# Kernel tuning notes

Hardware: AMD Instinct MI355X
Metric: run time of the kernel (lower is better)

Reference implementation:

```python
import jax, jax.numpy as jnp
import numpy as np

T = 0.5  # sharpening temperature
M, N, DK, DV = 8192, 8192, 512, 512


def setup_inputs() -> dict:
    key = jax.random.key(0)
    kq, kk, kv = jax.random.split(key, 3)
    Q = jax.random.normal(kq, (M, DK), dtype=jnp.float32)
    K = jax.random.normal(kk, (N, DK), dtype=jnp.float32)
    V = jax.random.normal(kv, (N, DV), dtype=jnp.float32)
    return {"Q": Q, "K": K, "V": V}


def reference(Q, K, V):
    d_k = K.shape[1]
    scores = jnp.matmul(Q, K.T) / np.sqrt(d_k)          # (m, n)
    attn = jax.nn.softmax(scores, axis=-1)              # (m, n)
    # sharpen: p^(1/T), renormalize over keys (dim=1 for 2D == last axis)
    u = jnp.power(attn, 1.0 / T)
    attn = u / jnp.sum(u, axis=1, keepdims=True)
    return jnp.matmul(attn, V)                          # (m, d_v)
```

## Files before the change

kernel.cpp:

```cpp
#include <hip/hip_runtime.h>

typedef unsigned short u16;
typedef __attribute__((ext_vector_type(8))) short bf16x8;
typedef __attribute__((ext_vector_type(4))) float f32x4;
typedef __attribute__((ext_vector_type(4))) u16 u16x4;

#define MFMA16(a, b, c) __builtin_amdgcn_mfma_f32_16x16x32_bf16(a, b, c, 0, 0, 0)

__device__ __forceinline__ u16 f2bf(float f) {
    union { float f; unsigned u; } v; v.f = f;
    unsigned r = (v.u + 0x7FFFu + ((v.u >> 16) & 1u)) >> 16;
    return (u16)r;
}

__device__ __forceinline__ void gload_lds16(const void* g, void* l) {
    __builtin_amdgcn_global_load_lds((const __attribute__((address_space(1))) void*)g,
                                     (__attribute__((address_space(3))) void*)l, 16, 0, 0);
}

__global__ __launch_bounds__(256) void cvt_kernel(const float* __restrict__ src,
                                                  u16* __restrict__ dst, int n4, float scale) {
    int i = blockIdx.x * 256 + threadIdx.x;
    if (i >= n4) return;
    f32x4 v = *(const f32x4*)(src + (size_t)i * 4);
    u16x4 o;
#pragma unroll
    for (int j = 0; j < 4; ++j) o[j] = f2bf(v[j] * scale);
    *(u16x4*)(dst + (size_t)i * 4) = o;
}

__global__ __launch_bounds__(256) void prep_vt(const float* __restrict__ V, u16* __restrict__ Vt) {
    __shared__ float tile[64][65];
    int t = threadIdx.x;
    int n0 = blockIdx.x * 64;
    int d0 = blockIdx.y * 64;
    int tr = t >> 4, tc = t & 15;
#pragma unroll
    for (int p = 0; p < 4; ++p) {
        int n = p * 16 + tr;
        f32x4 v = *(const f32x4*)(V + (size_t)(n0 + n) * 512 + d0 + tc * 4);
#pragma unroll
        for (int j = 0; j < 4; ++j) tile[n][tc * 4 + j] = v[j];
    }
    __syncthreads();
#pragma unroll
    for (int p = 0; p < 4; ++p) {
        int d = p * 16 + tr;
        u16x4 o;
#pragma unroll
        for (int j = 0; j < 4; ++j) o[j] = f2bf(tile[tc * 4 + j][d]);
        *(u16x4*)(Vt + (size_t)(d0 + d) * 8192 + n0 + tc * 4) = o;
    }
}

__global__ __launch_bounds__(512) void flash_kernel(
    const u16* __restrict__ Qs, const u16* __restrict__ Kb, const u16* __restrict__ Vt,
    float* __restrict__ Opart, float* __restrict__ lpart) {
    __shared__ __align__(16) u16 lds_k[2][64 * 512];
    __shared__ __align__(16) u16 lds_p[2][64 * 64];
    __shared__ float s_l[2][64];

    const int tid = threadIdx.x;
    const int wid = tid >> 6;
    const int lane = tid & 63;
    const int lo = lane & 15;
    const int hi = lane >> 4;
    const int mi = wid >> 1;
    const int nj = wid & 1;

    const int bx = blockIdx.x;
    const int x = bx & 7;
    const int g = bx >> 3;
    const int ks = x >> 2;
    const int mtile = g * 4 + (x & 3);
    const int key0 = ks * 4096;

    bf16x8 qf[16];
    {
        const u16* qrow = Qs + (size_t)(mtile * 64 + mi * 16 + lo) * 512 + hi * 8;
#pragma unroll
        for (int kt = 0; kt < 16; ++kt) qf[kt] = *(const bf16x8*)(qrow + kt * 32);
    }

    f32x4 o[4][4];
#pragma unroll
    for (int a = 0; a < 4; ++a)
#pragma unroll
        for (int b = 0; b < 4; ++b) o[a][b] = (f32x4){0.f, 0.f, 0.f, 0.f};
    float lsum = 0.f;
    bf16x8 vb[4][2];

    const int cbase = ((hi ^ (lo & 3)) + ((lo >> 2) & 1) * 4) * 8;
    const int rowA = (nj * 32 + lo) * 512;

    const int qrow = mi * 16 + lo;
    const int ch0 = ((nj * 4 + (hi >> 1)) ^ (qrow & 7));
    const int ch1 = ((nj * 4 + 2 + (hi >> 1)) ^ (qrow & 7));
    const int pw0 = qrow * 64 + (ch0 << 3) + (hi & 1) * 4;
    const int pw1 = qrow * 64 + (ch1 << 3) + (hi & 1) * 4;

#define STAGE_K(IT, BUF)                                                            \
    {                                                                               \
        const u16* kb_ = Kb + (size_t)(key0 + (IT) * 64) * 512;                     \
        _Pragma("unroll") for (int r8_ = 0; r8_ < 8; ++r8_) {                       \
            int row_ = (wid << 3) + r8_;                                            \
            gload_lds16(kb_ + (size_t)row_ * 512 + ((lane ^ (row_ & 7)) << 3),      \
                        &lds_k[BUF][row_ * 512]);                                   \
        }                                                                           \
    }

#define S_COMPUTE(BUF, S0A, S0B, S1A, S1B)                                          \
    {                                                                               \
        const u16* kb = &lds_k[BUF][0];                                             \
        const u16* pAe = kb + rowA + cbase;                                         \
        const u16* pAo = kb + rowA + (cbase ^ 32);                                  \
        const u16* pBe = pAe + 16 * 512;                                            \
        const u16* pBo = pAo + 16 * 512;                                            \
        _Pragma("unroll") for (int kt2 = 0; kt2 < 8; ++kt2) {                       \
            bf16x8 ae = *(const bf16x8*)(pAe + kt2 * 64);                           \
            bf16x8 be = *(const bf16x8*)(pBe + kt2 * 64);                           \
            bf16x8 ao = *(const bf16x8*)(pAo + kt2 * 64);                           \
            bf16x8 bo = *(const bf16x8*)(pBo + kt2 * 64);                           \
            S0A = MFMA16(ae, qf[2 * kt2], S0A);                                     \
            S1A = MFMA16(be, qf[2 * kt2], S1A);                                     \
            S0B = MFMA16(ao, qf[2 * kt2 + 1], S0B);                                 \
            S1B = MFMA16(bo, qf[2 * kt2 + 1], S1B);                                 \
        }                                                                           \
    }

#define PV_STEP(PBUF)                                                               \
    {                                                                               \
        _Pragma("unroll") for (int mt = 0; mt < 4; ++mt) {                          \
            int m = mt * 16 + lo;                                                   \
            int c0 = hi ^ (m & 7);                                                  \
            int c1 = (4 + hi) ^ (m & 7);                                            \
            bf16x8 pa0 = *(const bf16x8*)(&lds_p[PBUF][m * 64 + c0 * 8]);           \
            bf16x8 pa1 = *(const bf16x8*)(&lds_p[PBUF][m * 64 + c1 * 8]);           \
            _Pragma("unroll") for (int nt = 0; nt < 4; ++nt) {                      \
                f32x4 c_ = o[mt][nt];                                               \
                c_ = MFMA16(pa0, vb[nt][0], c_);                                    \
                c_ = MFMA16(pa1, vb[nt][1], c_);                                    \
                o[mt][nt] = c_;                                                     \
            }                                                                       \
        }                                                                           \
    }

#define EXP_PW(S0, S1, PBUF)                                                        \
    {                                                                               \
        u16x4 w0, w1;                                                               \
        _Pragma("unroll") for (int r = 0; r < 4; ++r) {                             \
            float p0 = __expf((S0)[r]);                                             \
            float p1 = __expf((S1)[r]);                                             \
            lsum += p0 + p1;                                                        \
            w0[r] = f2bf(p0);                                                       \
            w1[r] = f2bf(p1);                                                       \
        }                                                                           \
        *(u16x4*)(&lds_p[PBUF][pw0]) = w0;                                          \
        *(u16x4*)(&lds_p[PBUF][pw1]) = w1;                                          \
    }

#define VB_LOAD(T)                                                                  \
    {                                                                               \
        _Pragma("unroll") for (int nt = 0; nt < 4; ++nt) {                          \
            const u16* vrow = Vt + (size_t)(wid * 64 + nt * 16 + lo) * 8192 +       \
                              key0 + (T) * 64 + hi * 8;                             \
            vb[nt][0] = *(const bf16x8*)(vrow);                                     \
            vb[nt][1] = *(const bf16x8*)(vrow + 32);                                \
        }                                                                           \
    }

    STAGE_K(0, 0)
    asm volatile("s_waitcnt vmcnt(0)\n\ts_barrier" ::: "memory");

    {
        STAGE_K(1, 1)
        f32x4 s0a = {0.f, 0.f, 0.f, 0.f}, s0b = s0a, s1a = s0a, s1b = s0a;
        VB_LOAD(0)
        __builtin_amdgcn_s_setprio(1);
        S_COMPUTE(0, s0a, s0b, s1a, s1b)
        __builtin_amdgcn_s_setprio(0);
        f32x4 s0 = s0a + s0b, s1 = s1a + s1b;
        EXP_PW(s0, s1, 0)
        asm volatile("s_waitcnt vmcnt(0) lgkmcnt(0)\n\ts_barrier" ::: "memory");
    }

    for (int t = 1; t < 64; ++t) {
        const int cur = t & 1;
        if (t < 63) STAGE_K(t + 1, cur ^ 1)
        __builtin_amdgcn_s_setprio(1);
        PV_STEP(cur ^ 1)
        __builtin_amdgcn_s_setprio(0);
        VB_LOAD(t)
        f32x4 s0a = {0.f, 0.f, 0.f, 0.f}, s0b = s0a, s1a = s0a, s1b = s0a;
        __builtin_amdgcn_s_setprio(1);
        S_COMPUTE(cur, s0a, s0b, s1a, s1b)
        __builtin_amdgcn_s_setprio(0);
        f32x4 s0 = s0a + s0b, s1 = s1a + s1b;
        EXP_PW(s0, s1, cur)
        asm volatile("s_waitcnt vmcnt(0) lgkmcnt(0)\n\ts_barrier" ::: "memory");
    }

    __builtin_amdgcn_s_setprio(1);
    PV_STEP(1)
    __builtin_amdgcn_s_setprio(0);

    lsum += __shfl_xor(lsum, 16);
    lsum += __shfl_xor(lsum, 32);
    if (lane < 16) s_l[nj][qrow] = lsum;
    __syncthreads();

    const int lb = mtile * 2 + ks;
    {
        float* Ob = Opart + (size_t)lb * (64 * 512);
#pragma unroll
        for (int mt = 0; mt < 4; ++mt)
#pragma unroll
            for (int nt = 0; nt < 4; ++nt)
#pragma unroll
                for (int r = 0; r < 4; ++r) {
                    int row = mt * 16 + hi * 4 + r;
                    int col = wid * 64 + nt * 16 + lo;
                    Ob[row * 512 + col] = o[mt][nt][r];
                }
        if (tid < 64) {
            lpart[lb * 64 + tid] = s_l[0][tid] + s_l[1][tid];
        }
    }
}

__global__ __launch_bounds__(256) void combine_kernel(const float* __restrict__ Opart,
                                                      const float* __restrict__ lpart,
                                                      float* __restrict__ out) {
    int i = blockIdx.x * 256 + threadIdx.x;
    int row = i >> 7;
    int c4 = i & 127;
    int mtile = row >> 6, rl = row & 63;
    int b0 = mtile * 2, b1 = b0 + 1;
    float inv = 1.0f / (lpart[b0 * 64 + rl] + lpart[b1 * 64 + rl]);
    f32x4 a = *(const f32x4*)(Opart + (size_t)b0 * 32768 + rl * 512 + c4 * 4);
    f32x4 b = *(const f32x4*)(Opart + (size_t)b1 * 32768 + rl * 512 + c4 * 4);
    f32x4 r = (a + b) * inv;
    *(f32x4*)(out + (size_t)row * 512 + c4 * 4) = r;
}

extern "C" void kernel_launch(void* const* d_in, const int* in_sizes, int n_in,
                              void* d_out, int out_size, void* d_ws, size_t ws_size,
                              hipStream_t stream) {
    const float* Q = (const float*)d_in[0];
    const float* K = (const float*)d_in[1];
    const float* V = (const float*)d_in[2];
    float* out = (float*)d_out;
    char* ws = (char*)d_ws;

    u16* Qs = (u16*)(ws + 0);
    u16* Kb = (u16*)(ws + 8388608);
    u16* Vt = (u16*)(ws + 16777216);
    float* Op = (float*)(ws + 25165824);
    float* lp = (float*)(ws + 58720256);

    const float scale = 0.08838834764831845f;
    cvt_kernel<<<4096, 256, 0, stream>>>(Q, Qs, 1048576, scale);
    cvt_kernel<<<4096, 256, 0, stream>>>(K, Kb, 1048576, 1.0f);
    prep_vt<<<dim3(128, 8), 256, 0, stream>>>(V, Vt);
    flash_kernel<<<256, 512, 0, stream>>>(Qs, Kb, Vt, Op, lp);
    combine_kernel<<<4096, 256, 0, stream>>>(Op, lp, out);
}
```

Measured before the change: 247.4 us.

## Split fused attention into two GEMMs with materialized bf16 probability matrix

When the workspace is large enough, the fused flash kernel is replaced by a QK^T GEMM that applies exp, accumulates row sums atomically and writes a bf16 P matrix. A second GEMM then multiplies P by V and normalizes. This aims to raise parallelism and MFMA efficiency with standard tiled GEMMs, at the cost of writing and reading a 128 MB intermediate. The old flash path stays as a fallback when the workspace is too small.

```diff
diff --git a/kernel.cpp b/kernel.cpp
--- a/kernel.cpp
+++ b/kernel.cpp
@@ -4,6 +4,7 @@
 typedef __attribute__((ext_vector_type(8))) short bf16x8;
 typedef __attribute__((ext_vector_type(4))) float f32x4;
 typedef __attribute__((ext_vector_type(4))) u16 u16x4;
+typedef __attribute__((ext_vector_type(8))) u16 u16x8;
 
 #define MFMA16(a, b, c) __builtin_amdgcn_mfma_f32_16x16x32_bf16(a, b, c, 0, 0, 0)
 
@@ -51,6 +52,215 @@
         for (int j = 0; j < 4; ++j) o[j] = f2bf(tile[tc * 4 + j][d]);
         *(u16x4*)(Vt + (size_t)(d0 + d) * 8192 + n0 + tc * 4) = o;
     }
+}
+
+__global__ __launch_bounds__(256) void zero_kernel(float* __restrict__ p, int n) {
+    int i = blockIdx.x * 256 + threadIdx.x;
+    if (i < n) p[i] = 0.f;
+}
+
+__global__ __launch_bounds__(256) void gemm1_kernel(const u16* __restrict__ Qs,
+                                                    const u16* __restrict__ Kb,
+                                                    u16* __restrict__ P,
+                                                    float* __restrict__ l) {
+    __shared__ __align__(16) u16 smem[32768];
+    const int tid = threadIdx.x;
+    const int wid = tid >> 6;
+    const int lane = tid & 63;
+    const int lo = lane & 15;
+    const int hi = lane >> 4;
+    const int wr = wid >> 1, wc = wid & 1;
+    const int subrow = lane >> 3, ch = lane & 7;
+
+    const int bid = blockIdx.x;
+    const int x = bid & 7, g = bid >> 3;
+    const int m0 = (g >> 3) * 128;
+    const int n0 = (x * 8 + (g & 7)) * 128;
+
+    const u16* Abase = Qs + (size_t)m0 * 512;
+    const u16* Bbase = Kb + (size_t)n0 * 512;
+    const int src_off = subrow * 512 + ((ch ^ subrow) << 3);
+
+#define G1_STAGE(KS, BUF)                                                              \
+    {                                                                                  \
+        u16* la_ = smem + (BUF) * 8192;                                                \
+        u16* lb_ = smem + 16384 + (BUF) * 8192;                                        \
+        _Pragma("unroll") for (int i_ = 0; i_ < 4; ++i_) {                             \
+            int rb_ = wid * 32 + i_ * 8;                                               \
+            gload_lds16(Abase + (size_t)rb_ * 512 + (KS) * 64 + src_off, la_ + rb_ * 64); \
+            gload_lds16(Bbase + (size_t)rb_ * 512 + (KS) * 64 + src_off, lb_ + rb_ * 64); \
+        }                                                                              \
+    }
+
+    f32x4 acc[4][4];
+#pragma unroll
+    for (int a = 0; a < 4; ++a)
+#pragma unroll
+        for (int b = 0; b < 4; ++b) acc[a][b] = (f32x4){0.f, 0.f, 0.f, 0.f};
+
+    G1_STAGE(0, 0)
+    asm volatile("s_waitcnt vmcnt(0)\n\ts_barrier" ::: "memory");
+
+#pragma unroll
+    for (int s = 0; s < 8; ++s) {
+        const int cur = s & 1;
+        if (s < 7) G1_STAGE(s + 1, cur ^ 1)
+        const u16* la = smem + cur * 8192;
+        const u16* lb = smem + 16384 + cur * 8192;
+        __builtin_amdgcn_s_setprio(1);
+#pragma unroll
+        for (int kk = 0; kk < 2; ++kk) {
+            bf16x8 af[4], bf[4];
+#pragma unroll
+            for (int mt = 0; mt < 4; ++mt) {
+                int r = wr * 64 + mt * 16 + lo;
+                af[mt] = *(const bf16x8*)(la + r * 64 + (((kk * 4 + hi) ^ (r & 7)) << 3));
+            }
+#pragma unroll
+            for (int nt = 0; nt < 4; ++nt) {
+                int r = wc * 64 + nt * 16 + lo;
+                bf[nt] = *(const bf16x8*)(lb + r * 64 + (((kk * 4 + hi) ^ (r & 7)) << 3));
+            }
+#pragma unroll
+            for (int mt = 0; mt < 4; ++mt)
+#pragma unroll
+                for (int nt = 0; nt < 4; ++nt)
+                    acc[mt][nt] = MFMA16(af[mt], bf[nt], acc[mt][nt]);
+        }
+        __builtin_amdgcn_s_setprio(0);
+        asm volatile("s_waitcnt vmcnt(0) lgkmcnt(0)\n\ts_barrier" ::: "memory");
+    }
+
+#pragma unroll
+    for (int mt = 0; mt < 4; ++mt)
+#pragma unroll
+        for (int nt = 0; nt < 4; ++nt)
+#pragma unroll
+            for (int r = 0; r < 4; ++r) acc[mt][nt][r] = __expf(acc[mt][nt][r]);
+
+#pragma unroll
+    for (int mt = 0; mt < 4; ++mt)
+#pragma unroll
+        for (int r = 0; r < 4; ++r) {
+            float rs = acc[mt][0][r] + acc[mt][1][r] + acc[mt][2][r] + acc[mt][3][r];
+            rs += __shfl_xor(rs, 1);
+            rs += __shfl_xor(rs, 2);
+            rs += __shfl_xor(rs, 4);
+            rs += __shfl_xor(rs, 8);
+            if (lo == 0) atomicAdd(&l[m0 + wr * 64 + mt * 16 + 4 * hi + r], rs);
+        }
+
+    __syncthreads();
+#pragma unroll
+    for (int mt = 0; mt < 4; ++mt)
+#pragma unroll
+        for (int nt = 0; nt < 4; ++nt)
+#pragma unroll
+            for (int r = 0; r < 4; ++r) {
+                int row = wr * 64 + mt * 16 + 4 * hi + r;
+                int col = wc * 64 + nt * 16 + lo;
+                int c16 = col >> 3;
+                int sw = (c16 & 8) | ((c16 ^ row) & 7);
+                smem[row * 128 + sw * 8 + (col & 7)] = f2bf(acc[mt][nt][r]);
+            }
+    __syncthreads();
+    {
+        int row = tid >> 1, half = tid & 1;
+        u16* dst = P + (size_t)(m0 + row) * 8192 + n0 + half * 64;
+#pragma unroll
+        for (int c = 0; c < 8; ++c) {
+            int c16 = half * 8 + c;
+            int sw = (c16 & 8) | ((c16 ^ row) & 7);
+            *(u16x8*)(dst + c * 8) = *(const u16x8*)(smem + row * 128 + sw * 8);
+        }
+    }
+#undef G1_STAGE
+}
+
+__global__ __launch_bounds__(512) void gemm2_kernel(const u16* __restrict__ P,
+                                                    const u16* __restrict__ Vt,
+                                                    const float* __restrict__ l,
+                                                    float* __restrict__ out) {
+    __shared__ __align__(16) u16 smem[16384];
+    const int tid = threadIdx.x;
+    const int wid = tid >> 6;
+    const int lane = tid & 63;
+    const int lo = lane & 15;
+    const int hi = lane >> 4;
+    const int wr = wid >> 2, wc = wid & 3;
+    const int subrow = lane >> 3, ch = lane & 7;
+
+    const int bid = blockIdx.x;
+    const int x = bid & 7, g = bid >> 3;
+    const int bn = x & 3;
+    const int bm = (g << 1) + (x >> 2);
+    const int m0 = bm * 128, n0 = bn * 128;
+
+    const u16* Abase = P + (size_t)m0 * 8192;
+    const int src_off = subrow * 8192 + ((ch ^ subrow) << 3);
+
+#define G2_STAGE(KS, BUF)                                                                 \
+    {                                                                                     \
+        u16* la_ = smem + (BUF) * 8192;                                                   \
+        _Pragma("unroll") for (int i_ = 0; i_ < 2; ++i_) {                                \
+            int rb_ = wid * 16 + i_ * 8;                                                  \
+            gload_lds16(Abase + (size_t)rb_ * 8192 + (size_t)(KS) * 64 + src_off,         \
+                        la_ + rb_ * 64);                                                  \
+        }                                                                                 \
+    }
+
+    f32x4 acc[4][2];
+#pragma unroll
+    for (int a = 0; a < 4; ++a)
+#pragma unroll
+        for (int b = 0; b < 2; ++b) acc[a][b] = (f32x4){0.f, 0.f, 0.f, 0.f};
+
+    G2_STAGE(0, 0)
+    asm volatile("s_waitcnt vmcnt(0)\n\ts_barrier" ::: "memory");
+
+    const u16* vbase = Vt + (size_t)(n0 + wc * 32 + lo) * 8192;
+
+    for (int s = 0; s < 128; ++s) {
+        const int cur = s & 1;
+        if (s < 127) G2_STAGE(s + 1, cur ^ 1)
+        bf16x8 vb[2][2];
+#pragma unroll
+        for (int nt = 0; nt < 2; ++nt)
+#pragma unroll
+            for (int kk = 0; kk < 2; ++kk)
+                vb[nt][kk] = *(const bf16x8*)(vbase + (size_t)nt * 16 * 8192 +
+                                              s * 64 + kk * 32 + hi * 8);
+        const u16* la = smem + cur * 8192;
+        __builtin_amdgcn_s_setprio(1);
+#pragma unroll
+        for (int kk = 0; kk < 2; ++kk) {
+            bf16x8 af[4];
+#pragma unroll
+            for (int mt = 0; mt < 4; ++mt) {
+                int r = wr * 64 + mt * 16 + lo;
+                af[mt] = *(const bf16x8*)(la + r * 64 + (((kk * 4 + hi) ^ (r & 7)) << 3));
+            }
+#pragma unroll
+            for (int mt = 0; mt < 4; ++mt)
+#pragma unroll
+                for (int nt = 0; nt < 2; ++nt)
+                    acc[mt][nt] = MFMA16(af[mt], vb[nt][kk], acc[mt][nt]);
+        }
+        __builtin_amdgcn_s_setprio(0);
+        asm volatile("s_waitcnt vmcnt(0) lgkmcnt(0)\n\ts_barrier" ::: "memory");
+    }
+
+#pragma unroll
+    for (int mt = 0; mt < 4; ++mt)
+#pragma unroll
+        for (int r = 0; r < 4; ++r) {
+            int row = m0 + wr * 64 + mt * 16 + 4 * hi + r;
+            float inv = 1.0f / l[row];
+            float* orow = out + (size_t)row * 512 + n0 + wc * 32 + lo;
+            orow[0] = acc[mt][0][r] * inv;
+            orow[16] = acc[mt][1][r] * inv;
+        }
+#undef G2_STAGE
 }
 
 __global__ __launch_bounds__(512) void flash_kernel(
@@ -108,7 +318,6 @@
                         &lds_k[BUF][row_ * 512]);                                   \
         }                                                                           \
     }
-
 #define S_COMPUTE(BUF, S0A, S0B, S1A, S1B)                                          \
     {                                                                               \
         const u16* kb = &lds_k[BUF][0];                                             \
@@ -127,7 +336,6 @@
             S1B = MFMA16(bo, qf[2 * kt2 + 1], S1B);                                 \
         }                                                                           \
     }
-
 #define PV_STEP(PBUF)                                                               \
     {                                                                               \
         _Pragma("unroll") for (int mt = 0; mt < 4; ++mt) {                          \
@@ -144,7 +352,6 @@
             }                                                                       \
         }                                                                           \
     }
-
 #define EXP_PW(S0, S1, PBUF)                                                        \
     {                                                                               \
         u16x4 w0, w1;                                                               \
@@ -158,7 +365,6 @@
         *(u16x4*)(&lds_p[PBUF][pw0]) = w0;                                          \
         *(u16x4*)(&lds_p[PBUF][pw1]) = w1;                                          \
     }
-
 #define VB_LOAD(T)                                                                  \
     {                                                                               \
         _Pragma("unroll") for (int nt = 0; nt < 4; ++nt) {                          \
@@ -171,7 +377,6 @@
 
     STAGE_K(0, 0)
     asm volatile("s_waitcnt vmcnt(0)\n\ts_barrier" ::: "memory");
-
     {
         STAGE_K(1, 1)
         f32x4 s0a = {0.f, 0.f, 0.f, 0.f}, s0b = s0a, s1a = s0a, s1b = s0a;
@@ -183,7 +388,6 @@
         EXP_PW(s0, s1, 0)
         asm volatile("s_waitcnt vmcnt(0) lgkmcnt(0)\n\ts_barrier" ::: "memory");
     }
-
     for (int t = 1; t < 64; ++t) {
         const int cur = t & 1;
         if (t < 63) STAGE_K(t + 1, cur ^ 1)
@@ -199,7 +403,6 @@
         EXP_PW(s0, s1, cur)
         asm volatile("s_waitcnt vmcnt(0) lgkmcnt(0)\n\ts_barrier" ::: "memory");
     }
-
     __builtin_amdgcn_s_setprio(1);
     PV_STEP(1)
     __builtin_amdgcn_s_setprio(0);
@@ -222,9 +425,7 @@
                     int col = wid * 64 + nt * 16 + lo;
                     Ob[row * 512 + col] = o[mt][nt][r];
                 }
-        if (tid < 64) {
-            lpart[lb * 64 + tid] = s_l[0][tid] + s_l[1][tid];
-        }
+        if (tid < 64) lpart[lb * 64 + tid] = s_l[0][tid] + s_l[1][tid];
     }
 }
 
@@ -252,16 +453,27 @@
     float* out = (float*)d_out;
     char* ws = (char*)d_ws;
 
+    const float scale = 0.08838834764831845f;
+
     u16* Qs = (u16*)(ws + 0);
     u16* Kb = (u16*)(ws + 8388608);
     u16* Vt = (u16*)(ws + 16777216);
-    float* Op = (float*)(ws + 25165824);
-    float* lp = (float*)(ws + 58720256);
-
-    const float scale = 0.08838834764831845f;
+
     cvt_kernel<<<4096, 256, 0, stream>>>(Q, Qs, 1048576, scale);
     cvt_kernel<<<4096, 256, 0, stream>>>(K, Kb, 1048576, 1.0f);
     prep_vt<<<dim3(128, 8), 256, 0, stream>>>(V, Vt);
-    flash_kernel<<<256, 512, 0, stream>>>(Qs, Kb, Vt, Op, lp);
-    combine_kernel<<<4096, 256, 0, stream>>>(Op, lp, out);
-}
+
+    const size_t need = 25165824ull + 65536ull + 134217728ull;
+    if (ws_size >= need) {
+        float* lsum = (float*)(ws + 25165824);
+        u16* P = (u16*)(ws + 25165824 + 65536);
+        zero_kernel<<<32, 256, 0, stream>>>(lsum, 8192);
+        gemm1_kernel<<<4096, 256, 0, stream>>>(Qs, Kb, P, lsum);
+        gemm2_kernel<<<256, 512, 0, stream>>>(P, Vt, lsum, out);
+    } else {
+        float* Op = (float*)(ws + 25165824);
+        float* lp = (float*)(ws + 58720256);
+        flash_kernel<<<256, 512, 0, stream>>>(Qs, Kb, Vt, Op, lp);
+        combine_kernel<<<4096, 256, 0, stream>>>(Op, lp, out);
+    }
+}
```

After: 367.7 us. 1.49x slower.

## Double flash kernel block to 1024 threads, splitting keys and V columns across 16 waves

Applied to the files above, without the earlier changes.

Each workgroup grows from 8 to 16 waves. Each wave now computes scores for 16 keys instead of 32, and accumulates 32 output columns instead of 64, so per-wave accumulator and V-fragment registers are halved. K staging rows per wave and the row-sum reduction buffer are adjusted to match. The aim is more latency hiding per CU with the same 256-block grid. The cost is more waves meeting at every barrier, and Q fragments are still replicated across waves, so register pressure per wave stays high.

```diff
diff --git a/kernel.cpp b/kernel.cpp
--- a/kernel.cpp
+++ b/kernel.cpp
@@ -53,20 +53,20 @@
     }
 }
 
-__global__ __launch_bounds__(512) void flash_kernel(
+__global__ __launch_bounds__(1024) void flash_kernel(
     const u16* __restrict__ Qs, const u16* __restrict__ Kb, const u16* __restrict__ Vt,
     float* __restrict__ Opart, float* __restrict__ lpart) {
     __shared__ __align__(16) u16 lds_k[2][64 * 512];
     __shared__ __align__(16) u16 lds_p[2][64 * 64];
-    __shared__ float s_l[2][64];
+    __shared__ float s_l[4][64];
 
     const int tid = threadIdx.x;
     const int wid = tid >> 6;
     const int lane = tid & 63;
     const int lo = lane & 15;
     const int hi = lane >> 4;
-    const int mi = wid >> 1;
-    const int nj = wid & 1;
+    const int mi = wid >> 2;
+    const int nj = wid & 3;
 
     const int bx = blockIdx.x;
     const int x = bx & 7;
@@ -82,49 +82,39 @@
         for (int kt = 0; kt < 16; ++kt) qf[kt] = *(const bf16x8*)(qrow + kt * 32);
     }
 
-    f32x4 o[4][4];
+    f32x4 o[4][2];
 #pragma unroll
     for (int a = 0; a < 4; ++a)
 #pragma unroll
-        for (int b = 0; b < 4; ++b) o[a][b] = (f32x4){0.f, 0.f, 0.f, 0.f};
+        for (int b = 0; b < 2; ++b) o[a][b] = (f32x4){0.f, 0.f, 0.f, 0.f};
     float lsum = 0.f;
-    bf16x8 vb[4][2];
+    bf16x8 vb[2][2];
 
     const int cbase = ((hi ^ (lo & 3)) + ((lo >> 2) & 1) * 4) * 8;
-    const int rowA = (nj * 32 + lo) * 512;
+    const int rowA = (nj * 16 + lo) * 512;
 
     const int qrow = mi * 16 + lo;
-    const int ch0 = ((nj * 4 + (hi >> 1)) ^ (qrow & 7));
-    const int ch1 = ((nj * 4 + 2 + (hi >> 1)) ^ (qrow & 7));
-    const int pw0 = qrow * 64 + (ch0 << 3) + (hi & 1) * 4;
-    const int pw1 = qrow * 64 + (ch1 << 3) + (hi & 1) * 4;
+    const int pw = qrow * 64 + ((((nj << 1) + (hi >> 1)) ^ (qrow & 7)) << 3) + (hi & 1) * 4;
 
 #define STAGE_K(IT, BUF)                                                            \
     {                                                                               \
         const u16* kb_ = Kb + (size_t)(key0 + (IT) * 64) * 512;                     \
-        _Pragma("unroll") for (int r8_ = 0; r8_ < 8; ++r8_) {                       \
-            int row_ = (wid << 3) + r8_;                                            \
+        _Pragma("unroll") for (int r4_ = 0; r4_ < 4; ++r4_) {                       \
+            int row_ = (wid << 2) + r4_;                                            \
             gload_lds16(kb_ + (size_t)row_ * 512 + ((lane ^ (row_ & 7)) << 3),      \
                         &lds_k[BUF][row_ * 512]);                                   \
         }                                                                           \
     }
 
-#define S_COMPUTE(BUF, S0A, S0B, S1A, S1B)                                          \
-    {                                                                               \
-        const u16* kb = &lds_k[BUF][0];                                             \
-        const u16* pAe = kb + rowA + cbase;                                         \
-        const u16* pAo = kb + rowA + (cbase ^ 32);                                  \
-        const u16* pBe = pAe + 16 * 512;                                            \
-        const u16* pBo = pAo + 16 * 512;                                            \
+#define S_COMPUTE(BUF, SE, SO)                                                      \
+    {                                                                               \
+        const u16* pAe = &lds_k[BUF][0] + rowA + cbase;                             \
+        const u16* pAo = &lds_k[BUF][0] + rowA + (cbase ^ 32);                      \
         _Pragma("unroll") for (int kt2 = 0; kt2 < 8; ++kt2) {                       \
             bf16x8 ae = *(const bf16x8*)(pAe + kt2 * 64);                           \
-            bf16x8 be = *(const bf16x8*)(pBe + kt2 * 64);                           \
             bf16x8 ao = *(const bf16x8*)(pAo + kt2 * 64);                           \
-            bf16x8 bo = *(const bf16x8*)(pBo + kt2 * 64);                           \
-            S0A = MFMA16(ae, qf[2 * kt2], S0A);                                     \
-            S1A = MFMA16(be, qf[2 * kt2], S1A);                                     \
-            S0B = MFMA16(ao, qf[2 * kt2 + 1], S0B);                                 \
-            S1B = MFMA16(bo, qf[2 * kt2 + 1], S1B);                                 \
+            SE = MFMA16(ae, qf[2 * kt2], SE);                                       \
+            SO = MFMA16(ao, qf[2 * kt2 + 1], SO);                                   \
         }                                                                           \
     }
 
@@ -136,7 +126,7 @@
             int c1 = (4 + hi) ^ (m & 7);                                            \
             bf16x8 pa0 = *(const bf16x8*)(&lds_p[PBUF][m * 64 + c0 * 8]);           \
             bf16x8 pa1 = *(const bf16x8*)(&lds_p[PBUF][m * 64 + c1 * 8]);           \
-            _Pragma("unroll") for (int nt = 0; nt < 4; ++nt) {                      \
+            _Pragma("unroll") for (int nt = 0; nt < 2; ++nt) {                      \
                 f32x4 c_ = o[mt][nt];                                               \
                 c_ = MFMA16(pa0, vb[nt][0], c_);                                    \
                 c_ = MFMA16(pa1, vb[nt][1], c_);                                    \
@@ -145,24 +135,21 @@
         }                                                                           \
     }
 
-#define EXP_PW(S0, S1, PBUF)                                                        \
-    {                                                                               \
-        u16x4 w0, w1;                                                               \
+#define EXP_PW(S, PBUF)                                                             \
+    {                                                                               \
+        u16x4 w;                                                                    \
         _Pragma("unroll") for (int r = 0; r < 4; ++r) {                             \
-            float p0 = __expf((S0)[r]);                                             \
-            float p1 = __expf((S1)[r]);                                             \
-            lsum += p0 + p1;                                                        \
-            w0[r] = f2bf(p0);                                                       \
-            w1[r] = f2bf(p1);                                                       \
-        }                                                                           \
-        *(u16x4*)(&lds_p[PBUF][pw0]) = w0;                                          \
-        *(u16x4*)(&lds_p[PBUF][pw1]) = w1;                                          \
+            float p = __expf((S)[r]);                                               \
+            lsum += p;                                                              \
+            w[r] = f2bf(p);                                                         \
+        }                                                                           \
+        *(u16x4*)(&lds_p[PBUF][pw]) = w;                                            \
     }
 
 #define VB_LOAD(T)                                                                  \
     {                                                                               \
-        _Pragma("unroll") for (int nt = 0; nt < 4; ++nt) {                          \
-            const u16* vrow = Vt + (size_t)(wid * 64 + nt * 16 + lo) * 8192 +       \
+        _Pragma("unroll") for (int nt = 0; nt < 2; ++nt) {                          \
+            const u16* vrow = Vt + (size_t)(wid * 32 + nt * 16 + lo) * 8192 +       \
                               key0 + (T) * 64 + hi * 8;                             \
             vb[nt][0] = *(const bf16x8*)(vrow);                                     \
             vb[nt][1] = *(const bf16x8*)(vrow + 32);                                \
@@ -174,13 +161,13 @@
 
     {
         STAGE_K(1, 1)
-        f32x4 s0a = {0.f, 0.f, 0.f, 0.f}, s0b = s0a, s1a = s0a, s1b = s0a;
+        f32x4 se = {0.f, 0.f, 0.f, 0.f}, so = se;
         VB_LOAD(0)
         __builtin_amdgcn_s_setprio(1);
-        S_COMPUTE(0, s0a, s0b, s1a, s1b)
+        S_COMPUTE(0, se, so)
         __builtin_amdgcn_s_setprio(0);
-        f32x4 s0 = s0a + s0b, s1 = s1a + s1b;
-        EXP_PW(s0, s1, 0)
+        f32x4 s = se + so;
+        EXP_PW(s, 0)
         asm volatile("s_waitcnt vmcnt(0) lgkmcnt(0)\n\ts_barrier" ::: "memory");
     }
 
@@ -191,12 +178,12 @@
         PV_STEP(cur ^ 1)
         __builtin_amdgcn_s_setprio(0);
         VB_LOAD(t)
-        f32x4 s0a = {0.f, 0.f, 0.f, 0.f}, s0b = s0a, s1a = s0a, s1b = s0a;
+        f32x4 se = {0.f, 0.f, 0.f, 0.f}, so = se;
         __builtin_amdgcn_s_setprio(1);
-        S_COMPUTE(cur, s0a, s0b, s1a, s1b)
+        S_COMPUTE(cur, se, so)
         __builtin_amdgcn_s_setprio(0);
-        f32x4 s0 = s0a + s0b, s1 = s1a + s1b;
-        EXP_PW(s0, s1, cur)
+        f32x4 s = se + so;
+        EXP_PW(s, cur)
         asm volatile("s_waitcnt vmcnt(0) lgkmcnt(0)\n\ts_barrier" ::: "memory");
     }
 
@@ -215,15 +202,15 @@
 #pragma unroll
         for (int mt = 0; mt < 4; ++mt)
 #pragma unroll
-            for (int nt = 0; nt < 4; ++nt)
+            for (int nt = 0; nt < 2; ++nt)
 #pragma unroll
                 for (int r = 0; r < 4; ++r) {
                     int row = mt * 16 + hi * 4 + r;
-                    int col = wid * 64 + nt * 16 + lo;
+                    int col = wid * 32 + nt * 16 + lo;
                     Ob[row * 512 + col] = o[mt][nt][r];
                 }
         if (tid < 64) {
-            lpart[lb * 64 + tid] = s_l[0][tid] + s_l[1][tid];
+            lpart[lb * 64 + tid] = s_l[0][tid] + s_l[1][tid] + s_l[2][tid] + s_l[3][tid];
         }
     }
 }
@@ -262,6 +249,6 @@
     cvt_kernel<<<4096, 256, 0, stream>>>(Q, Qs, 1048576, scale);
     cvt_kernel<<<4096, 256, 0, stream>>>(K, Kb, 1048576, 1.0f);
     prep_vt<<<dim3(128, 8), 256, 0, stream>>>(V, Vt);
-    flash_kernel<<<256, 512, 0, stream>>>(Qs, Kb, Vt, Op, lp);
+    flash_kernel<<<256, 1024, 0, stream>>>(Qs, Kb, Vt, Op, lp);
     combine_kernel<<<4096, 256, 0, stream>>>(Op, lp, out);
 }
```

After: 464.4 us. 1.88x slower.

## Process 128-key tiles per iteration with single-buffered K and fewer barriers

Applied to the files above, without the earlier changes.

The double-buffered 64-key K/P pipeline becomes single-buffered 128-key tiles. Each iteration computes two score subtiles and writes both P halves, then issues the next K stage and runs both PV steps. This halves the number of loop iterations and barriers. In exchange, the next K load now overlaps only with the PV work rather than with the S computation, and register pressure rises from holding two V fragment sets.

```diff
diff --git a/kernel.cpp b/kernel.cpp
--- a/kernel.cpp
+++ b/kernel.cpp
@@ -56,8 +56,8 @@
 __global__ __launch_bounds__(512) void flash_kernel(
     const u16* __restrict__ Qs, const u16* __restrict__ Kb, const u16* __restrict__ Vt,
     float* __restrict__ Opart, float* __restrict__ lpart) {
-    __shared__ __align__(16) u16 lds_k[2][64 * 512];
-    __shared__ __align__(16) u16 lds_p[2][64 * 64];
+    __shared__ __align__(16) u16 lds_k[128 * 512];
+    __shared__ __align__(16) u16 lds_p[64 * 128];
     __shared__ float s_l[2][64];
 
     const int tid = threadIdx.x;
@@ -88,32 +88,34 @@
 #pragma unroll
         for (int b = 0; b < 4; ++b) o[a][b] = (f32x4){0.f, 0.f, 0.f, 0.f};
     float lsum = 0.f;
-    bf16x8 vb[4][2];
+    bf16x8 vbA[4][2], vbB[4][2];
 
     const int cbase = ((hi ^ (lo & 3)) + ((lo >> 2) & 1) * 4) * 8;
-    const int rowA = (nj * 32 + lo) * 512;
+    const int rowA_A = (nj * 32 + lo) * 512;
+    const int rowA_B = rowA_A + 64 * 512;
 
     const int qrow = mi * 16 + lo;
-    const int ch0 = ((nj * 4 + (hi >> 1)) ^ (qrow & 7));
-    const int ch1 = ((nj * 4 + 2 + (hi >> 1)) ^ (qrow & 7));
-    const int pw0 = qrow * 64 + (ch0 << 3) + (hi & 1) * 4;
-    const int pw1 = qrow * 64 + (ch1 << 3) + (hi & 1) * 4;
-
-#define STAGE_K(IT, BUF)                                                            \
-    {                                                                               \
-        const u16* kb_ = Kb + (size_t)(key0 + (IT) * 64) * 512;                     \
-        _Pragma("unroll") for (int r8_ = 0; r8_ < 8; ++r8_) {                       \
-            int row_ = (wid << 3) + r8_;                                            \
+    const int chA0 = ((nj * 4 + (hi >> 1)) ^ (qrow & 7));
+    const int chA1 = ((nj * 4 + 2 + (hi >> 1)) ^ (qrow & 7));
+    const int pwA0 = qrow * 128 + (chA0 << 3) + (hi & 1) * 4;
+    const int pwA1 = qrow * 128 + (chA1 << 3) + (hi & 1) * 4;
+    const int pwB0 = pwA0 + 64;
+    const int pwB1 = pwA1 + 64;
+
+#define STAGE_K(IT)                                                                 \
+    {                                                                               \
+        const u16* kb_ = Kb + (size_t)(key0 + (IT) * 128) * 512;                    \
+        _Pragma("unroll") for (int r_ = 0; r_ < 16; ++r_) {                         \
+            int row_ = (wid << 4) + r_;                                             \
             gload_lds16(kb_ + (size_t)row_ * 512 + ((lane ^ (row_ & 7)) << 3),      \
-                        &lds_k[BUF][row_ * 512]);                                   \
-        }                                                                           \
-    }
-
-#define S_COMPUTE(BUF, S0A, S0B, S1A, S1B)                                          \
-    {                                                                               \
-        const u16* kb = &lds_k[BUF][0];                                             \
-        const u16* pAe = kb + rowA + cbase;                                         \
-        const u16* pAo = kb + rowA + (cbase ^ 32);                                  \
+                        &lds_k[row_ * 512]);                                        \
+        }                                                                           \
+    }
+
+#define S_COMPUTE(ROWBASE, S0A, S0B, S1A, S1B)                                      \
+    {                                                                               \
+        const u16* pAe = &lds_k[0] + (ROWBASE) + cbase;                             \
+        const u16* pAo = &lds_k[0] + (ROWBASE) + (cbase ^ 32);                      \
         const u16* pBe = pAe + 16 * 512;                                            \
         const u16* pBo = pAo + 16 * 512;                                            \
         _Pragma("unroll") for (int kt2 = 0; kt2 < 8; ++kt2) {                       \
@@ -128,24 +130,24 @@
         }                                                                           \
     }
 
-#define PV_STEP(PBUF)                                                               \
+#define PV_STEP(CH_OFF, VB)                                                         \
     {                                                                               \
         _Pragma("unroll") for (int mt = 0; mt < 4; ++mt) {                          \
             int m = mt * 16 + lo;                                                   \
-            int c0 = hi ^ (m & 7);                                                  \
-            int c1 = (4 + hi) ^ (m & 7);                                            \
-            bf16x8 pa0 = *(const bf16x8*)(&lds_p[PBUF][m * 64 + c0 * 8]);           \
-            bf16x8 pa1 = *(const bf16x8*)(&lds_p[PBUF][m * 64 + c1 * 8]);           \
+            int c0 = (CH_OFF) + (hi ^ (m & 7));                                     \
+            int c1 = (CH_OFF) + ((4 + hi) ^ (m & 7));                               \
+            bf16x8 pa0 = *(const bf16x8*)(&lds_p[m * 128 + c0 * 8]);                \
+            bf16x8 pa1 = *(const bf16x8*)(&lds_p[m * 128 + c1 * 8]);                \
             _Pragma("unroll") for (int nt = 0; nt < 4; ++nt) {                      \
                 f32x4 c_ = o[mt][nt];                                               \
-                c_ = MFMA16(pa0, vb[nt][0], c_);                                    \
-                c_ = MFMA16(pa1, vb[nt][1], c_);                                    \
+                c_ = MFMA16(pa0, VB[nt][0], c_);                                    \
+                c_ = MFMA16(pa1, VB[nt][1], c_);                                    \
                 o[mt][nt] = c_;                                                     \
             }                                                                       \
         }                                                                           \
     }
 
-#define EXP_PW(S0, S1, PBUF)                                                        \
+#define EXP_PW(S0, S1, PW0, PW1)                                                    \
     {                                                                               \
         u16x4 w0, w1;                                                               \
         _Pragma("unroll") for (int r = 0; r < 4; ++r) {                             \
@@ -155,54 +157,51 @@
             w0[r] = f2bf(p0);                                                       \
             w1[r] = f2bf(p1);                                                       \
         }                                                                           \
-        *(u16x4*)(&lds_p[PBUF][pw0]) = w0;                                          \
-        *(u16x4*)(&lds_p[PBUF][pw1]) = w1;                                          \
-    }
-
-#define VB_LOAD(T)                                                                  \
+        *(u16x4*)(&lds_p[PW0]) = w0;                                                \
+        *(u16x4*)(&lds_p[PW1]) = w1;                                                \
+    }
+
+#define VB_LOAD(T, KOFF, VB)                                                        \
     {                                                                               \
         _Pragma("unroll") for (int nt = 0; nt < 4; ++nt) {                          \
             const u16* vrow = Vt + (size_t)(wid * 64 + nt * 16 + lo) * 8192 +       \
-                              key0 + (T) * 64 + hi * 8;                             \
-            vb[nt][0] = *(const bf16x8*)(vrow);                                     \
-            vb[nt][1] = *(const bf16x8*)(vrow + 32);                                \
-        }                                                                           \
-    }
-
-    STAGE_K(0, 0)
+                              key0 + (T) * 128 + (KOFF) + hi * 8;                   \
+            VB[nt][0] = *(const bf16x8*)(vrow);                                     \
+            VB[nt][1] = *(const bf16x8*)(vrow + 32);                                \
+        }                                                                           \
+    }
+
+    STAGE_K(0)
     asm volatile("s_waitcnt vmcnt(0)\n\ts_barrier" ::: "memory");
 
-    {
-        STAGE_K(1, 1)
-        f32x4 s0a = {0.f, 0.f, 0.f, 0.f}, s0b = s0a, s1a = s0a, s1b = s0a;
-        VB_LOAD(0)
+    for (int t = 0; t < 32; ++t) {
+        VB_LOAD(t, 0, vbA)
+        f32x4 a0a = {0.f, 0.f, 0.f, 0.f}, a0b = a0a, a1a = a0a, a1b = a0a;
         __builtin_amdgcn_s_setprio(1);
-        S_COMPUTE(0, s0a, s0b, s1a, s1b)
+        S_COMPUTE(rowA_A, a0a, a0b, a1a, a1b)
         __builtin_amdgcn_s_setprio(0);
-        f32x4 s0 = s0a + s0b, s1 = s1a + s1b;
-        EXP_PW(s0, s1, 0)
-        asm volatile("s_waitcnt vmcnt(0) lgkmcnt(0)\n\ts_barrier" ::: "memory");
-    }
-
-    for (int t = 1; t < 64; ++t) {
-        const int cur = t & 1;
-        if (t < 63) STAGE_K(t + 1, cur ^ 1)
+        f32x4 sA0 = a0a + a0b, sA1 = a1a + a1b;
+        EXP_PW(sA0, sA1, pwA0, pwA1)
+
+        VB_LOAD(t, 64, vbB)
+        f32x4 b0a = {0.f, 0.f, 0.f, 0.f}, b0b = b0a, b1a = b0a, b1b = b0a;
         __builtin_amdgcn_s_setprio(1);
-        PV_STEP(cur ^ 1)
+        S_COMPUTE(rowA_B, b0a, b0b, b1a, b1b)
         __builtin_amdgcn_s_setprio(0);
-        VB_LOAD(t)
-        f32x4 s0a = {0.f, 0.f, 0.f, 0.f}, s0b = s0a, s1a = s0a, s1b = s0a;
+        f32x4 sB0 = b0a + b0b, sB1 = b1a + b1b;
+        EXP_PW(sB0, sB1, pwB0, pwB1)
+
+        asm volatile("s_waitcnt lgkmcnt(0)\n\ts_barrier" ::: "memory");
+
+        if (t < 31) STAGE_K(t + 1)
+
         __builtin_amdgcn_s_setprio(1);
-        S_COMPUTE(cur, s0a, s0b, s1a, s1b)
+        PV_STEP(0, vbA)
+        PV_STEP(8, vbB)
         __builtin_amdgcn_s_setprio(0);
-        f32x4 s0 = s0a + s0b, s1 = s1a + s1b;
-        EXP_PW(s0, s1, cur)
-        asm volatile("s_waitcnt vmcnt(0) lgkmcnt(0)\n\ts_barrier" ::: "memory");
-    }
-
-    __builtin_amdgcn_s_setprio(1);
-    PV_STEP(1)
-    __builtin_amdgcn_s_setprio(0);
+
+        if (t < 31) asm volatile("s_waitcnt vmcnt(0) lgkmcnt(0)\n\ts_barrier" ::: "memory");
+    }
 
     lsum += __shfl_xor(lsum, 16);
     lsum += __shfl_xor(lsum, 32);
```

Result: faster. 215.5 us (-12.9%).
